# Optimization experiments

Measured on AMD Instinct MI355X. Metric: run time of the kernel, lower is better.

## Reference

```python
import math
import jax, jax.numpy as jnp
import numpy as np

B, LD, LE = 4, 1024, 1024
D, H, DK, DV, DFF, NL = 256, 8, 32, 32, 1024, 6


def _fixed_pos_emb(L, d):
    inv_freq = 1.0 / (10000.0 ** (jnp.arange(0, d, 2, dtype=jnp.float32) / d))
    pos = jnp.arange(L, dtype=jnp.float32)
    s = pos[:, None] * inv_freq[None, :]          # [L, d/2]
    return jnp.concatenate([jnp.sin(s), jnp.cos(s)], axis=-1)  # [L, d]


def _ln(x, g, b, eps=1e-5):
    m = x.mean(-1, keepdims=True)
    v = x.var(-1, keepdims=True)
    return (x - m) / jnp.sqrt(v + eps) * g + b


def _mha(x_q, x_kv, Wq, bq, Wk, bk, Wv, bv, Wo, bo, g, b, mask):
    Bq, Lq, _ = x_q.shape
    q = (x_q @ Wq + bq).reshape(Bq, Lq, H, DK).transpose(0, 2, 1, 3)   # [B,H,Lq,DK]
    k = (x_kv @ Wk + bk).reshape(Bq, -1, H, DK).transpose(0, 2, 1, 3)  # [B,H,Lk,DK]
    v = (x_kv @ Wv + bv).reshape(Bq, -1, H, DV).transpose(0, 2, 1, 3)  # [B,H,Lk,DV]
    scores = jnp.einsum('bhqd,bhkd->bhqk', q, k) / math.sqrt(DK)
    scores = jnp.where(mask[:, None, :, :], -1e9, scores)
    attn = jax.nn.softmax(scores, axis=-1)
    ctx = jnp.einsum('bhqk,bhkd->bhqd', attn, v)
    ctx = ctx.transpose(0, 2, 1, 3).reshape(Bq, Lq, H * DV)
    return _ln(ctx @ Wo + bo + x_q, g, b)


def _ffn(x, W1, b1, W2, b2, g, b):
    h = jax.nn.relu(x @ W1 + b1)   # conv1d k=1 == pointwise linear
    return _ln(h @ W2 + b2 + x, g, b)


def setup_inputs() -> dict:
    key = jax.random.key(0)
    ks = iter(jax.random.split(key, 40))
    def p(shape):
        return jax.random.normal(next(ks), shape, jnp.float32) * 0.02
    inp = {
        'enc_outputs': jax.random.normal(next(ks), (B, LE, D), jnp.float32),
        'dec_inputs': jax.random.normal(next(ks), (B, LD, 3), jnp.float32),
        'enc_masks': jnp.zeros((B, LE), jnp.int32),
        'dec_masks': jnp.zeros((B, LD), jnp.int32),
        'W_tgt': p((3, D)), 'b_tgt': jnp.zeros((D,), jnp.float32),
        'sa_Wq': p((NL, D, H * DK)), 'sa_bq': jnp.zeros((NL, H * DK), jnp.float32),
        'sa_Wk': p((NL, D, H * DK)), 'sa_bk': jnp.zeros((NL, H * DK), jnp.float32),
        'sa_Wv': p((NL, D, H * DV)), 'sa_bv': jnp.zeros((NL, H * DV), jnp.float32),
        'sa_Wo': p((NL, H * DV, D)), 'sa_bo': jnp.zeros((NL, D), jnp.float32),
        'sa_ln_g': jnp.ones((NL, D), jnp.float32), 'sa_ln_b': jnp.zeros((NL, D), jnp.float32),
        'ca_Wq': p((NL, D, H * DK)), 'ca_bq': jnp.zeros((NL, H * DK), jnp.float32),
        'ca_Wk': p((NL, D, H * DK)), 'ca_bk': jnp.zeros((NL, H * DK), jnp.float32),
        'ca_Wv': p((NL, D, H * DV)), 'ca_bv': jnp.zeros((NL, H * DV), jnp.float32),
        'ca_Wo': p((NL, H * DV, D)), 'ca_bo': jnp.zeros((NL, D), jnp.float32),
        'ca_ln_g': jnp.ones((NL, D), jnp.float32), 'ca_ln_b': jnp.zeros((NL, D), jnp.float32),
        'ff_W1': p((NL, D, DFF)), 'ff_b1': jnp.zeros((NL, DFF), jnp.float32),
        'ff_W2': p((NL, DFF, D)), 'ff_b2': jnp.zeros((NL, D), jnp.float32),
        'ff_ln_g': jnp.ones((NL, D), jnp.float32), 'ff_ln_b': jnp.zeros((NL, D), jnp.float32),
    }
    return inp


def reference(enc_outputs, dec_inputs, enc_masks, dec_masks, W_tgt, b_tgt,
              sa_Wq, sa_bq, sa_Wk, sa_bk, sa_Wv, sa_bv, sa_Wo, sa_bo, sa_ln_g, sa_ln_b,
              ca_Wq, ca_bq, ca_Wk, ca_bk, ca_Wv, ca_bv, ca_Wo, ca_bo, ca_ln_g, ca_ln_b,
              ff_W1, ff_b1, ff_W2, ff_b2, ff_ln_g, ff_ln_b):
    x = dec_inputs @ W_tgt + b_tgt                                  # tgt_emb
    pad = dec_masks[:, None, :].astype(bool)                        # [B,1,LD]
    causal = jnp.triu(jnp.ones((LD, LD), bool), 1)[None]            # [1,LD,LD]
    self_mask = pad | causal                                        # [B,LD,LD]
    cross_mask = jnp.broadcast_to(enc_masks[:, None, :].astype(bool), (x.shape[0], LD, LE))
    pe = _fixed_pos_emb(LD, D)[None]                                # [1,LD,D]
    for i in range(NL):
        x = x + pe                                                  # pos emb applied every layer (as in source)
        x = _mha(x, x, sa_Wq[i], sa_bq[i], sa_Wk[i], sa_bk[i], sa_Wv[i], sa_bv[i],
                 sa_Wo[i], sa_bo[i], sa_ln_g[i], sa_ln_b[i], self_mask)
        x = _mha(x, enc_outputs, ca_Wq[i], ca_bq[i], ca_Wk[i], ca_bk[i], ca_Wv[i], ca_bv[i],
                 ca_Wo[i], ca_bo[i], ca_ln_g[i], ca_ln_b[i], cross_mask)
        x = _ffn(x, ff_W1[i], ff_b1[i], ff_W2[i], ff_b2[i], ff_ln_g[i], ff_ln_b[i])
    return x
```

## Files before the change

kernel.cpp:

```cpp
#include <hip/hip_runtime.h>
#include <hip/hip_bf16.h>

#define B_   4
#define LD_  1024
#define LE_  1024
#define D_   256
#define H_   8
#define DK_  32
#define DFF_ 1024
#define NL_  6
#define NTOK (B_ * LD_)
#define M1E  1048576

typedef __hip_bfloat16 bf16;
typedef __bf16 bf16_t;
typedef bf16_t bf16x8 __attribute__((ext_vector_type(8)));
typedef bf16_t bf16x4 __attribute__((ext_vector_type(4)));
typedef float  f32x4  __attribute__((ext_vector_type(4)));

__device__ __forceinline__ float bits2f(unsigned short u) {
    union { unsigned int i; float f; } w; w.i = ((unsigned int)u) << 16; return w.f;
}
__device__ __forceinline__ float ldx(const void* p, size_t i, int f32) {
    if (f32) return ((const float*)p)[i];
    return bits2f(((const unsigned short*)p)[i]);
}

__global__ __launch_bounds__(256) void detect_kernel(
    const void* __restrict__ enc, int* __restrict__ flag)
{
    __shared__ int bad;
    if (threadIdx.x == 0) bad = 0;
    __syncthreads();
    const unsigned short* u = (const unsigned short*)enc;
    int b = 0;
    for (int i = threadIdx.x; i < 4096; i += 256) {
        unsigned short e = (u[i] >> 7) & 0xFF;
        if (e >= 142) b = 1;
    }
    if (b) atomicOr(&bad, 1);
    __syncthreads();
    if (threadIdx.x == 0) *flag = bad;
}

__global__ __launch_bounds__(256) void pe_build_kernel(float* __restrict__ pe)
{
    int i = blockIdx.x * 256 + threadIdx.x;
    int d = i & (D_ - 1);
    int pos = i >> 8;
    int j = d & 127;
    float inv = powf(10000.0f, -2.0f * (float)j / (float)D_);
    float s = (float)pos * inv;
    pe[i] = (d < 128) ? sinf(s) : cosf(s);
}

__global__ __launch_bounds__(256) void embed_kernel(
    const void* __restrict__ dec, const void* __restrict__ Wt,
    const void* __restrict__ bt, float* __restrict__ x,
    const float* __restrict__ pe, const int* __restrict__ flag)
{
    int f32 = *flag;
    int i = blockIdx.x * 256 + threadIdx.x;
    int d = i & (D_ - 1);
    int t = i >> 8;
    float a0 = ldx(dec, t * 3 + 0, f32);
    float a1 = ldx(dec, t * 3 + 1, f32);
    float a2 = ldx(dec, t * 3 + 2, f32);
    x[i] = ldx(bt, d, f32) + a0 * ldx(Wt, 0 * D_ + d, f32)
         + a1 * ldx(Wt, 1 * D_ + d, f32) + a2 * ldx(Wt, 2 * D_ + d, f32)
         + pe[i & (LD_ * D_ - 1)];
}

__global__ __launch_bounds__(256) void conv_kernel(
    const void* __restrict__ in, float* __restrict__ out, const int* __restrict__ flag)
{
    int f32 = *flag;
    int i = blockIdx.x * 256 + threadIdx.x;
    out[i] = ldx(in, i, f32);
}

__global__ __launch_bounds__(256) void gemm3_kernel(
    const float* __restrict__ A0, const float* __restrict__ A1, const float* __restrict__ A2,
    const void* __restrict__ W0, const void* __restrict__ W1, const void* __restrict__ W2,
    const void* __restrict__ bias0, const void* __restrict__ bias1, const void* __restrict__ bias2,
    float* __restrict__ C0, float* __restrict__ C1, float* __restrict__ C2,
    size_t wOff, size_t bOff,
    int M, int N, int K, int relu, int mode, const int* __restrict__ flag)
{
    const int f32 = *flag;
    const int z = blockIdx.z;
    const float* A = (z == 0) ? A0 : (z == 1) ? A1 : A2;
    const void*  W = (z == 0) ? W0 : (z == 1) ? W1 : W2;
    const void*  bias = (z == 0) ? bias0 : (z == 1) ? bias1 : bias2;
    float* C = (z == 0) ? C0 : (z == 1) ? C1 : C2;

    __shared__ __align__(16) bf16_t Ahi[32][40];
    __shared__ __align__(16) bf16_t Alo[32][40];
    __shared__ __align__(16) bf16_t Whi[64][40];
    __shared__ __align__(16) bf16_t Wlo[64][40];

    const int tid = threadIdx.x;
    const int m0 = blockIdx.y * 32, n0 = blockIdx.x * 64;
    const int w = tid >> 6, l = tid & 63, l15 = l & 15, lg = l >> 4;
    const int wr = w >> 1, wc = w & 1;

    const int ar = tid >> 3, ac = (tid & 7) * 4;
    const int wn = tid & 63, wkg = tid >> 6;
    const int wkb = 8 * (wkg ^ ((wn >> 3) & 3));

    const int fa = 16 * wr + l15;
    const int c0 = 32 * wc + l15, c1 = c0 + 16;
    const int kb0 = 8 * (lg ^ ((c0 >> 3) & 3));
    const int kb1 = 8 * (lg ^ ((c1 >> 3) & 3));

    f32x4 acc0 = {0.f, 0.f, 0.f, 0.f};
    f32x4 acc1 = {0.f, 0.f, 0.f, 0.f};

    float4 av = *(const float4*)&A[(size_t)(m0 + ar) * K + ac];
    float wf[8];
#pragma unroll
    for (int j = 0; j < 8; ++j)
        wf[j] = ldx(W, wOff + (size_t)(8 * wkg + j) * N + n0 + wn, f32);

    for (int k0 = 0; k0 < K; k0 += 32) {
        __syncthreads();
        {
            float af[4] = {av.x, av.y, av.z, av.w};
            bf16x4 h4, l4;
#pragma unroll
            for (int j = 0; j < 4; ++j) {
                bf16_t hv = (bf16_t)af[j];
                h4[j] = hv;
                l4[j] = (bf16_t)(af[j] - (float)hv);
            }
            *(bf16x4*)&Ahi[ar][ac] = h4;
            *(bf16x4*)&Alo[ar][ac] = l4;
            bf16x8 h8;
#pragma unroll
            for (int j = 0; j < 8; ++j) h8[j] = (bf16_t)wf[j];
            *(bf16x8*)&Whi[wn][wkb] = h8;
            if (f32) {
                bf16x8 l8;
#pragma unroll
                for (int j = 0; j < 8; ++j) l8[j] = (bf16_t)(wf[j] - (float)((bf16_t)wf[j]));
                *(bf16x8*)&Wlo[wn][wkb] = l8;
            }
        }
        __syncthreads();

        if (k0 + 32 < K) {
            av = *(const float4*)&A[(size_t)(m0 + ar) * K + k0 + 32 + ac];
#pragma unroll
            for (int j = 0; j < 8; ++j)
                wf[j] = ldx(W, wOff + (size_t)(k0 + 32 + 8 * wkg + j) * N + n0 + wn, f32);
        }

        bf16x8 ah = *(const bf16x8*)&Ahi[fa][8 * lg];
        bf16x8 al = *(const bf16x8*)&Alo[fa][8 * lg];
        bf16x8 bh0 = *(const bf16x8*)&Whi[c0][kb0];
        bf16x8 bh1 = *(const bf16x8*)&Whi[c1][kb1];
        acc0 = __builtin_amdgcn_mfma_f32_16x16x32_bf16(ah, bh0, acc0, 0, 0, 0);
        acc0 = __builtin_amdgcn_mfma_f32_16x16x32_bf16(al, bh0, acc0, 0, 0, 0);
        acc1 = __builtin_amdgcn_mfma_f32_16x16x32_bf16(ah, bh1, acc1, 0, 0, 0);
        acc1 = __builtin_amdgcn_mfma_f32_16x16x32_bf16(al, bh1, acc1, 0, 0, 0);
        if (f32) {
            bf16x8 bl0 = *(const bf16x8*)&Wlo[c0][kb0];
            bf16x8 bl1 = *(const bf16x8*)&Wlo[c1][kb1];
            acc0 = __builtin_amdgcn_mfma_f32_16x16x32_bf16(ah, bl0, acc0, 0, 0, 0);
            acc1 = __builtin_amdgcn_mfma_f32_16x16x32_bf16(ah, bl1, acc1, 0, 0, 0);
        }
    }

    const int cm = m0 + 16 * wr + 4 * lg;
    const int cn = n0 + 32 * wc + l15;
    const float b0v = ldx(bias, bOff + cn, f32);
    const float b1v = ldx(bias, bOff + cn + 16, f32);
    if (mode == 0) {
#pragma unroll
        for (int r = 0; r < 4; ++r) {
            float v0 = acc0[r] + b0v;
            float v1 = acc1[r] + b1v;
            if (relu) { v0 = fmaxf(v0, 0.f); v1 = fmaxf(v1, 0.f); }
            C[(size_t)(cm + r) * N + cn]      = v0;
            C[(size_t)(cm + r) * N + cn + 16] = v1;
        }
    } else {
        bf16_t* Cb = (bf16_t*)C;
        const float qs = (z == 0) ? 0.17677669529663687f : 1.0f;
#pragma unroll
        for (int r = 0; r < 4; ++r) {
            const int token = cm + r;
#pragma unroll
            for (int cc = 0; cc < 2; ++cc) {
                const int d = cn + 16 * cc;
                const float v = ((cc == 0 ? acc0[r] : acc1[r]) + (cc == 0 ? b0v : b1v)) * qs;
                if (z < 2) {
                    int bb = token >> 10, qw = (token >> 4) & 63, lt = token & 15;
                    int hh = d >> 5, lg2 = (d >> 3) & 3, jj = d & 7;
                    size_t base = ((size_t)((bb * 8 + hh) * 64 + qw)) * 1024
                                + (size_t)(lg2 * 16 + lt) * 8 + jj;
                    bf16_t hv = (bf16_t)v;
                    Cb[base]       = hv;
                    Cb[base + 512] = (bf16_t)(v - (float)hv);
                } else {
                    int bb = token >> 10, ktt = (token >> 6) & 15, c2 = (token >> 5) & 1;
                    int w32 = token & 31;
                    int lg2 = (w32 >> 2) & 3, jj = (w32 >> 4) * 4 + (w32 & 3);
                    int hh = d >> 5, dvh = (d >> 4) & 1, lt = d & 15;
                    size_t base = ((size_t)((bb * 8 + hh) * 16 + ktt)) * 2048
                                + c2 * 1024 + dvh * 512 + (size_t)(lg2 * 16 + lt) * 8 + jj;
                    Cb[base] = (bf16_t)v;
                }
            }
        }
    }
}

__global__ __launch_bounds__(256) void fattn4_kernel(
    const bf16_t* __restrict__ Qf, const bf16_t* __restrict__ Kf,
    const bf16_t* __restrict__ Vf, float* __restrict__ O,
    const int* __restrict__ mask, int causal)
{
    const int tid = threadIdx.x;
    const int qt = blockIdx.x, h = blockIdx.y, b = blockIdx.z;
    const int w = tid >> 6, l = tid & 63, l15 = l & 15, lg = l >> 4;
    const int bh = b * H_ + h;

    const size_t qbase = ((size_t)(bh * 64 + qt * 4 + w)) * 1024 + l * 8;
    const bf16x8 qh = *(const bf16x8*)(Qf + qbase);
    const bf16x8 ql = *(const bf16x8*)(Qf + qbase + 512);
    const int q_global = qt * 64 + w * 16 + l15;

    const bf16_t* kp = Kf + (size_t)bh * 64 * 1024 + l * 8;
    const bf16_t* vp = Vf + (size_t)bh * 16 * 2048 + l * 8;
    const int*    mp = mask + b * 1024 + 4 * lg;

    float m = -3.0e38f, lsum = 0.0f;
    f32x4 o0 = {0.f, 0.f, 0.f, 0.f};
    f32x4 o1 = {0.f, 0.f, 0.f, 0.f};

    const int nkt = causal ? (qt + 1) : (LE_ / 64);

    bf16x8 kha[4], kla[4], vaa[4];  int4 mka[4];
    bf16x8 khb[4], klb[4], vab[4];  int4 mkb[4];

#define FA_LOAD(kh_, kl_, va_, mk_, KT) do {                                    \
    _Pragma("unroll")                                                           \
    for (int nt = 0; nt < 4; ++nt) {                                            \
        kh_[nt] = *(const bf16x8*)(kp + (size_t)(KT) * 4096 + nt * 1024);       \
        kl_[nt] = *(const bf16x8*)(kp + (size_t)(KT) * 4096 + nt * 1024 + 512); \
    }                                                                           \
    va_[0] = *(const bf16x8*)(vp + (size_t)(KT) * 2048);                        \
    va_[1] = *(const bf16x8*)(vp + (size_t)(KT) * 2048 + 1024);                 \
    va_[2] = *(const bf16x8*)(vp + (size_t)(KT) * 2048 + 512);                  \
    va_[3] = *(const bf16x8*)(vp + (size_t)(KT) * 2048 + 1536);                 \
    _Pragma("unroll")                                                           \
    for (int nt = 0; nt < 4; ++nt)                                              \
        mk_[nt] = *(const int4*)(mp + (KT) * 64 + nt * 16);                     \
} while (0)

#define FA_COMPUTE(kh_, kl_, va_, mk_, KT) do {                                 \
    f32x4 s[4];                                                                 \
    _Pragma("unroll")                                                           \
    for (int nt = 0; nt < 4; ++nt) {                                            \
        f32x4 acc = {0.f, 0.f, 0.f, 0.f};                                       \
        acc = __builtin_amdgcn_mfma_f32_16x16x32_bf16(kh_[nt], qh, acc, 0,0,0); \
        acc = __builtin_amdgcn_mfma_f32_16x16x32_bf16(kl_[nt], qh, acc, 0,0,0); \
        acc = __builtin_amdgcn_mfma_f32_16x16x32_bf16(kh_[nt], ql, acc, 0,0,0); \
        s[nt] = acc;                                                            \
    }                                                                           \
    float pm = -3.0e38f;                                                        \
    _Pragma("unroll")                                                           \
    for (int nt = 0; nt < 4; ++nt) {                                            \
        _Pragma("unroll")                                                       \
        for (int r = 0; r < 4; ++r) {                                           \
            int key = (KT) * 64 + 16 * nt + 4 * lg + r;                         \
            int mv = (r==0)?mk_[nt].x:(r==1)?mk_[nt].y:(r==2)?mk_[nt].z:mk_[nt].w; \
            bool dead = (mv != 0) || (causal && key > q_global);                \
            float v = dead ? -1e30f : s[nt][r];                                 \
            s[nt][r] = v;                                                       \
            pm = fmaxf(pm, v);                                                  \
        }                                                                       \
    }                                                                           \
    pm = fmaxf(pm, __shfl_xor(pm, 16));                                         \
    pm = fmaxf(pm, __shfl_xor(pm, 32));                                         \
    float mnew = fmaxf(m, pm);                                                  \
    float alpha = __expf(m - mnew);                                             \
    m = mnew;                                                                   \
    float psum = 0.f;                                                           \
    _Pragma("unroll")                                                           \
    for (int nt = 0; nt < 4; ++nt) {                                            \
        _Pragma("unroll")                                                       \
        for (int r = 0; r < 4; ++r) {                                           \
            float p = __expf(s[nt][r] - m);                                     \
            s[nt][r] = p;                                                       \
            psum += p;                                                          \
        }                                                                       \
    }                                                                           \
    psum += __shfl_xor(psum, 16);                                               \
    psum += __shfl_xor(psum, 32);                                               \
    lsum = lsum * alpha + psum;                                                 \
    _Pragma("unroll")                                                           \
    for (int r = 0; r < 4; ++r) { o0[r] *= alpha; o1[r] *= alpha; }             \
    bf16x8 pb0, pb1;                                                            \
    _Pragma("unroll")                                                           \
    for (int r = 0; r < 4; ++r) {                                               \
        pb0[r]     = (bf16_t)s[0][r];  pb0[4 + r] = (bf16_t)s[1][r];            \
        pb1[r]     = (bf16_t)s[2][r];  pb1[4 + r] = (bf16_t)s[3][r];            \
    }                                                                           \
    o0 = __builtin_amdgcn_mfma_f32_16x16x32_bf16(va_[0], pb0, o0, 0, 0, 0);     \
    o0 = __builtin_amdgcn_mfma_f32_16x16x32_bf16(va_[1], pb1, o0, 0, 0, 0);     \
    o1 = __builtin_amdgcn_mfma_f32_16x16x32_bf16(va_[2], pb0, o1, 0, 0, 0);     \
    o1 = __builtin_amdgcn_mfma_f32_16x16x32_bf16(va_[3], pb1, o1, 0, 0, 0);     \
} while (0)

    FA_LOAD(kha, kla, vaa, mka, 0);
    int kt = 0;
    for (; kt + 2 <= nkt; kt += 2) {
        FA_LOAD(khb, klb, vab, mkb, kt + 1);
        FA_COMPUTE(kha, kla, vaa, mka, kt);
        if (kt + 2 < nkt) FA_LOAD(kha, kla, vaa, mka, kt + 2);
        FA_COMPUTE(khb, klb, vab, mkb, kt + 1);
    }
    if (kt < nkt) FA_COMPUTE(kha, kla, vaa, mka, kt);

#undef FA_LOAD
#undef FA_COMPUTE

    const float inv = 1.0f / lsum;
    float* op = O + ((size_t)(b * LD_ + q_global)) * D_ + h * DK_ + 4 * lg;
    f32x4 r0, r1;
#pragma unroll
    for (int r = 0; r < 4; ++r) { r0[r] = o0[r] * inv; r1[r] = o1[r] * inv; }
    *(f32x4*)op = r0;
    *(f32x4*)(op + 16) = r1;
}

__global__ __launch_bounds__(256) void ln_res_kernel(
    const float* __restrict__ t, float* __restrict__ x,
    const void* __restrict__ g, const void* __restrict__ bt,
    size_t gbOff, const float* __restrict__ pe, int addpe,
    const int* __restrict__ flag)
{
    int f32 = *flag;
    int tok = blockIdx.x * 4 + (threadIdx.x >> 6);
    int l = threadIdx.x & 63;
    size_t base = (size_t)tok * D_ + 4 * l;
    f32x4 tv = *(const f32x4*)(t + base);
    f32x4 xv = *(const f32x4*)(x + base);
    f32x4 v;
    float s1 = 0.f, s2 = 0.f;
#pragma unroll
    for (int j = 0; j < 4; ++j) {
        v[j] = tv[j] + xv[j];
        s1 += v[j];
        s2 += v[j] * v[j];
    }
#pragma unroll
    for (int off = 1; off < 64; off <<= 1) {
        s1 += __shfl_xor(s1, off);
        s2 += __shfl_xor(s2, off);
    }
    float mean = s1 * (1.0f / 256.0f);
    float var  = s2 * (1.0f / 256.0f) - mean * mean;
    float inv  = 1.0f / sqrtf(var + 1e-5f);
    f32x4 out;
#pragma unroll
    for (int j = 0; j < 4; ++j)
        out[j] = (v[j] - mean) * inv * ldx(g, gbOff + 4 * l + j, f32)
               + ldx(bt, gbOff + 4 * l + j, f32);
    if (addpe) {
        size_t pbase = (size_t)(tok & (LD_ - 1)) * D_ + 4 * l;
        f32x4 pv = *(const f32x4*)(pe + pbase);
#pragma unroll
        for (int j = 0; j < 4; ++j) out[j] += pv[j];
    }
    *(f32x4*)(x + base) = out;
}

__global__ __launch_bounds__(256) void cast_kernel(
    const float* __restrict__ x, void* __restrict__ out, const int* __restrict__ flag)
{
    int f32 = *flag;
    int i = blockIdx.x * 256 + threadIdx.x;
    if (f32) ((float*)out)[i] = x[i];
    else ((bf16*)out)[i] = __float2bfloat16(x[i]);
}

extern "C" void kernel_launch(void* const* d_in, const int* in_sizes, int n_in,
                              void* d_out, int out_size, void* d_ws, size_t ws_size,
                              hipStream_t stream)
{
    const void* enc       = d_in[0];
    const void* dec       = d_in[1];
    const int*  enc_masks = (const int*)d_in[2];
    const int*  dec_masks = (const int*)d_in[3];
    const void* W_tgt = d_in[4];
    const void* b_tgt = d_in[5];
    const void* sa_Wq = d_in[6];
    const void* sa_bq = d_in[7];
    const void* sa_Wk = d_in[8];
    const void* sa_bk = d_in[9];
    const void* sa_Wv = d_in[10];
    const void* sa_bv = d_in[11];
    const void* sa_Wo = d_in[12];
    const void* sa_bo = d_in[13];
    const void* sa_ln_g = d_in[14];
    const void* sa_ln_b = d_in[15];
    const void* ca_Wq = d_in[16];
    const void* ca_bq = d_in[17];
    const void* ca_Wk = d_in[18];
    const void* ca_bk = d_in[19];
    const void* ca_Wv = d_in[20];
    const void* ca_bv = d_in[21];
    const void* ca_Wo = d_in[22];
    const void* ca_bo = d_in[23];
    const void* ca_ln_g = d_in[24];
    const void* ca_ln_b = d_in[25];
    const void* ff_W1 = d_in[26];
    const void* ff_b1 = d_in[27];
    const void* ff_W2 = d_in[28];
    const void* ff_b2 = d_in[29];
    const void* ff_ln_g = d_in[30];
    const void* ff_ln_b = d_in[31];

    const size_t M1 = (size_t)NTOK * D_;
    float* ws = (float*)d_ws;
    float* x     = ws;
    float* t     = ws + 1 * M1;
    float* ctx   = ws + 2 * M1;
    float* enc_f = ws + 3 * M1;
    float* h     = ws + 4 * M1;
    bf16_t* qbuf = (bf16_t*)(ws + 4 * M1);
    bf16_t* kbuf = (bf16_t*)(ws + 5 * M1);
    bf16_t* vtbuf= (bf16_t*)(ws + 6 * M1);
    float* pe    = ws + 8 * M1;
    int*   flag  = (int*)(ws + 9 * M1);

    const int nElem = NTOK * D_;

    detect_kernel<<<1, 256, 0, stream>>>(enc, flag);
    pe_build_kernel<<<(LD_ * D_) / 256, 256, 0, stream>>>(pe);
    embed_kernel<<<nElem / 256, 256, 0, stream>>>(dec, W_tgt, b_tgt, x, pe, flag);
    conv_kernel<<<nElem / 256, 256, 0, stream>>>(enc, enc_f, flag);

    dim3 gProj(D_ / 64, NTOK / 32, 3);
    dim3 gOne(D_ / 64, NTOK / 32, 1);
    dim3 gFF1(DFF_ / 64, NTOK / 32, 1);
    dim3 gAttn(LD_ / 64, H_, B_);

    for (int i = 0; i < NL_; ++i) {
        const size_t wOff  = (size_t)i * D_ * D_;
        const size_t bOff  = (size_t)i * D_;
        const size_t f1Off = (size_t)i * D_ * DFF_;
        const size_t f1bOff= (size_t)i * DFF_;

        gemm3_kernel<<<gProj, 256, 0, stream>>>(
            x, x, x, sa_Wq, sa_Wk, sa_Wv, sa_bq, sa_bk, sa_bv,
            (float*)qbuf, (float*)kbuf, (float*)vtbuf,
            wOff, bOff, NTOK, D_, D_, 0, 1, flag);
        fattn4_kernel<<<gAttn, 256, 0, stream>>>(qbuf, kbuf, vtbuf, ctx, dec_masks, 1);
        gemm3_kernel<<<gOne, 256, 0, stream>>>(
            ctx, ctx, ctx, sa_Wo, sa_Wo, sa_Wo, sa_bo, sa_bo, sa_bo,
            t, t, t, wOff, bOff, NTOK, D_, D_, 0, 0, flag);
        ln_res_kernel<<<NTOK / 4, 256, 0, stream>>>(t, x, sa_ln_g, sa_ln_b, bOff, pe, 0, flag);

        gemm3_kernel<<<gProj, 256, 0, stream>>>(
            x, enc_f, enc_f, ca_Wq, ca_Wk, ca_Wv, ca_bq, ca_bk, ca_bv,
            (float*)qbuf, (float*)kbuf, (float*)vtbuf,
            wOff, bOff, NTOK, D_, D_, 0, 1, flag);
        fattn4_kernel<<<gAttn, 256, 0, stream>>>(qbuf, kbuf, vtbuf, ctx, enc_masks, 0);
        gemm3_kernel<<<gOne, 256, 0, stream>>>(
            ctx, ctx, ctx, ca_Wo, ca_Wo, ca_Wo, ca_bo, ca_bo, ca_bo,
            t, t, t, wOff, bOff, NTOK, D_, D_, 0, 0, flag);
        ln_res_kernel<<<NTOK / 4, 256, 0, stream>>>(t, x, ca_ln_g, ca_ln_b, bOff, pe, 0, flag);

        gemm3_kernel<<<gFF1, 256, 0, stream>>>(
            x, x, x, ff_W1, ff_W1, ff_W1, ff_b1, ff_b1, ff_b1,
            h, h, h, f1Off, f1bOff, NTOK, DFF_, D_, 1, 0, flag);
        gemm3_kernel<<<gOne, 256, 0, stream>>>(
            h, h, h, ff_W2, ff_W2, ff_W2, ff_b2, ff_b2, ff_b2,
            t, t, t, f1Off, bOff, NTOK, D_, DFF_, 0, 0, flag);
        ln_res_kernel<<<NTOK / 4, 256, 0, stream>>>(
            t, x, ff_ln_g, ff_ln_b, bOff, pe, (i < NL_ - 1) ? 1 : 0, flag);
    }

    cast_kernel<<<nElem / 256, 256, 0, stream>>>(x, d_out, flag);
}
```

Measured before the change: 1.100 ms.

## Fuse output projection GEMM with residual LayerNorm; skip A-lo pass for bf16 enc inputs

Adds a gemmln kernel in which each 1024-thread block computes a full 256-wide row tile of 16 tokens. It adds bias and residual and performs the LayerNorm reduction in-kernel, replacing the separate GEMM plus ln_res launches and the round trip through the t buffer. Each block reloads all of W for its K range, and a 16-row tile with 1024 threads may give lower MFMA efficiency than the earlier 32x64 tiles. It also drops the low-order split of the A operand for cross-attention K/V projections when inputs are bf16, since the encoder activations are exactly representable. It swizzles the query-tile order for attention blocks to balance the causal load.

Result: no change. 1.107 ms (+0.6%).

```diff
diff --git a/kernel.cpp b/kernel.cpp
--- a/kernel.cpp
+++ b/kernel.cpp
@@ -85,7 +85,7 @@
     const void* __restrict__ bias0, const void* __restrict__ bias1, const void* __restrict__ bias2,
     float* __restrict__ C0, float* __restrict__ C1, float* __restrict__ C2,
     size_t wOff, size_t bOff,
-    int M, int N, int K, int relu, int mode, const int* __restrict__ flag)
+    int M, int N, int K, int relu, int mode, int aexact, const int* __restrict__ flag)
 {
     const int f32 = *flag;
     const int z = blockIdx.z;
@@ -93,6 +93,7 @@
     const void*  W = (z == 0) ? W0 : (z == 1) ? W1 : W2;
     const void*  bias = (z == 0) ? bias0 : (z == 1) ? bias1 : bias2;
     float* C = (z == 0) ? C0 : (z == 1) ? C1 : C2;
+    const int ax = (!f32 && aexact && z > 0);
 
     __shared__ __align__(16) bf16_t Ahi[32][40];
     __shared__ __align__(16) bf16_t Alo[32][40];
@@ -134,7 +135,7 @@
                 l4[j] = (bf16_t)(af[j] - (float)hv);
             }
             *(bf16x4*)&Ahi[ar][ac] = h4;
-            *(bf16x4*)&Alo[ar][ac] = l4;
+            if (!ax) *(bf16x4*)&Alo[ar][ac] = l4;
             bf16x8 h8;
 #pragma unroll
             for (int j = 0; j < 8; ++j) h8[j] = (bf16_t)wf[j];
@@ -156,13 +157,15 @@
         }
 
         bf16x8 ah = *(const bf16x8*)&Ahi[fa][8 * lg];
-        bf16x8 al = *(const bf16x8*)&Alo[fa][8 * lg];
         bf16x8 bh0 = *(const bf16x8*)&Whi[c0][kb0];
         bf16x8 bh1 = *(const bf16x8*)&Whi[c1][kb1];
         acc0 = __builtin_amdgcn_mfma_f32_16x16x32_bf16(ah, bh0, acc0, 0, 0, 0);
-        acc0 = __builtin_amdgcn_mfma_f32_16x16x32_bf16(al, bh0, acc0, 0, 0, 0);
         acc1 = __builtin_amdgcn_mfma_f32_16x16x32_bf16(ah, bh1, acc1, 0, 0, 0);
-        acc1 = __builtin_amdgcn_mfma_f32_16x16x32_bf16(al, bh1, acc1, 0, 0, 0);
+        if (!ax) {
+            bf16x8 al = *(const bf16x8*)&Alo[fa][8 * lg];
+            acc0 = __builtin_amdgcn_mfma_f32_16x16x32_bf16(al, bh0, acc0, 0, 0, 0);
+            acc1 = __builtin_amdgcn_mfma_f32_16x16x32_bf16(al, bh1, acc1, 0, 0, 0);
+        }
         if (f32) {
             bf16x8 bl0 = *(const bf16x8*)&Wlo[c0][kb0];
             bf16x8 bl1 = *(const bf16x8*)&Wlo[c1][kb1];
@@ -216,13 +219,145 @@
     }
 }
 
+__global__ __launch_bounds__(1024) void gemmln_kernel(
+    const float* __restrict__ A, const void* __restrict__ W,
+    const void* __restrict__ bias, float* __restrict__ x,
+    const void* __restrict__ g, const void* __restrict__ bt,
+    size_t wOff, size_t bOff, int K,
+    const float* __restrict__ pe, int addpe, const int* __restrict__ flag)
+{
+    const int f32 = *flag;
+    __shared__ __align__(16) bf16_t Ahi[16][40];
+    __shared__ __align__(16) bf16_t Alo[16][40];
+    __shared__ __align__(16) bf16_t Whi[256][40];
+    __shared__ __align__(16) bf16_t Wlo[256][40];
+    __shared__ float red1[16][16];
+    __shared__ float red2[16][16];
+    __shared__ float mrow[16], irow[16];
+
+    const int tid = threadIdx.x;
+    const int m0 = blockIdx.x * 16;
+    const int w = tid >> 6, l = tid & 63, l15 = l & 15, lg = l >> 4;
+
+    const int ar = tid >> 3, ac = (tid & 7) * 4;
+    const int wn = tid & 255, wkg = tid >> 8;
+    const int wkb = 8 * (wkg ^ ((wn >> 3) & 3));
+    const int c = 16 * w + l15;
+    const int kb = 8 * (lg ^ ((c >> 3) & 3));
+
+    f32x4 acc = {0.f, 0.f, 0.f, 0.f};
+
+    float4 av;
+    float wf[8];
+    if (tid < 128) av = *(const float4*)&A[(size_t)(m0 + ar) * K + ac];
+#pragma unroll
+    for (int j = 0; j < 8; ++j)
+        wf[j] = ldx(W, wOff + (size_t)(8 * wkg + j) * 256 + wn, f32);
+
+    for (int k0 = 0; k0 < K; k0 += 32) {
+        __syncthreads();
+        if (tid < 128) {
+            float af[4] = {av.x, av.y, av.z, av.w};
+            bf16x4 h4, l4;
+#pragma unroll
+            for (int j = 0; j < 4; ++j) {
+                bf16_t hv = (bf16_t)af[j];
+                h4[j] = hv;
+                l4[j] = (bf16_t)(af[j] - (float)hv);
+            }
+            *(bf16x4*)&Ahi[ar][ac] = h4;
+            *(bf16x4*)&Alo[ar][ac] = l4;
+        }
+        {
+            bf16x8 h8;
+#pragma unroll
+            for (int j = 0; j < 8; ++j) h8[j] = (bf16_t)wf[j];
+            *(bf16x8*)&Whi[wn][wkb] = h8;
+            if (f32) {
+                bf16x8 l8;
+#pragma unroll
+                for (int j = 0; j < 8; ++j) l8[j] = (bf16_t)(wf[j] - (float)((bf16_t)wf[j]));
+                *(bf16x8*)&Wlo[wn][wkb] = l8;
+            }
+        }
+        __syncthreads();
+
+        if (k0 + 32 < K) {
+            if (tid < 128) av = *(const float4*)&A[(size_t)(m0 + ar) * K + k0 + 32 + ac];
+#pragma unroll
+            for (int j = 0; j < 8; ++j)
+                wf[j] = ldx(W, wOff + (size_t)(k0 + 32 + 8 * wkg + j) * 256 + wn, f32);
+        }
+
+        bf16x8 ah = *(const bf16x8*)&Ahi[l15][8 * lg];
+        bf16x8 bh = *(const bf16x8*)&Whi[c][kb];
+        acc = __builtin_amdgcn_mfma_f32_16x16x32_bf16(ah, bh, acc, 0, 0, 0);
+        {
+            bf16x8 al = *(const bf16x8*)&Alo[l15][8 * lg];
+            acc = __builtin_amdgcn_mfma_f32_16x16x32_bf16(al, bh, acc, 0, 0, 0);
+        }
+        if (f32) {
+            bf16x8 bl = *(const bf16x8*)&Wlo[c][kb];
+            acc = __builtin_amdgcn_mfma_f32_16x16x32_bf16(ah, bl, acc, 0, 0, 0);
+        }
+    }
+
+    const float bv = ldx(bias, bOff + c, f32);
+    f32x4 v;
+    float s1[4], s2[4];
+#pragma unroll
+    for (int r = 0; r < 4; ++r) {
+        int tok = m0 + 4 * lg + r;
+        v[r] = acc[r] + bv + x[(size_t)tok * 256 + c];
+        s1[r] = v[r];
+        s2[r] = v[r] * v[r];
+    }
+#pragma unroll
+    for (int r = 0; r < 4; ++r) {
+        s1[r] += __shfl_xor(s1[r], 1);  s2[r] += __shfl_xor(s2[r], 1);
+        s1[r] += __shfl_xor(s1[r], 2);  s2[r] += __shfl_xor(s2[r], 2);
+        s1[r] += __shfl_xor(s1[r], 4);  s2[r] += __shfl_xor(s2[r], 4);
+        s1[r] += __shfl_xor(s1[r], 8);  s2[r] += __shfl_xor(s2[r], 8);
+    }
+    if (l15 == 0) {
+#pragma unroll
+        for (int r = 0; r < 4; ++r) {
+            red1[w][4 * lg + r] = s1[r];
+            red2[w][4 * lg + r] = s2[r];
+        }
+    }
+    __syncthreads();
+    if (tid < 16) {
+        float t1 = 0.f, t2 = 0.f;
+#pragma unroll
+        for (int ww = 0; ww < 16; ++ww) { t1 += red1[ww][tid]; t2 += red2[ww][tid]; }
+        float mean = t1 * (1.0f / 256.0f);
+        float var  = t2 * (1.0f / 256.0f) - mean * mean;
+        mrow[tid] = mean;
+        irow[tid] = 1.0f / sqrtf(var + 1e-5f);
+    }
+    __syncthreads();
+
+    const float gv  = ldx(g,  bOff + c, f32);
+    const float btv = ldx(bt, bOff + c, f32);
+#pragma unroll
+    for (int r = 0; r < 4; ++r) {
+        int row = 4 * lg + r;
+        int tok = m0 + row;
+        float out = (v[r] - mrow[row]) * irow[row] * gv + btv;
+        if (addpe) out += pe[(size_t)(tok & (LD_ - 1)) * 256 + c];
+        x[(size_t)tok * 256 + c] = out;
+    }
+}
+
 __global__ __launch_bounds__(256) void fattn4_kernel(
     const bf16_t* __restrict__ Qf, const bf16_t* __restrict__ Kf,
     const bf16_t* __restrict__ Vf, float* __restrict__ O,
     const int* __restrict__ mask, int causal)
 {
     const int tid = threadIdx.x;
-    const int qt = blockIdx.x, h = blockIdx.y, b = blockIdx.z;
+    const int qt = (int)blockIdx.x ^ ((((int)blockIdx.z >> 1) & 1) << 3);
+    const int h = blockIdx.y, b = blockIdx.z;
     const int w = tid >> 6, l = tid & 63, l15 = l & 15, lg = l >> 4;
     const int bh = b * H_ + h;
 
@@ -334,48 +469,6 @@
     for (int r = 0; r < 4; ++r) { r0[r] = o0[r] * inv; r1[r] = o1[r] * inv; }
     *(f32x4*)op = r0;
     *(f32x4*)(op + 16) = r1;
-}
-
-__global__ __launch_bounds__(256) void ln_res_kernel(
-    const float* __restrict__ t, float* __restrict__ x,
-    const void* __restrict__ g, const void* __restrict__ bt,
-    size_t gbOff, const float* __restrict__ pe, int addpe,
-    const int* __restrict__ flag)
-{
-    int f32 = *flag;
-    int tok = blockIdx.x * 4 + (threadIdx.x >> 6);
-    int l = threadIdx.x & 63;
-    size_t base = (size_t)tok * D_ + 4 * l;
-    f32x4 tv = *(const f32x4*)(t + base);
-    f32x4 xv = *(const f32x4*)(x + base);
-    f32x4 v;
-    float s1 = 0.f, s2 = 0.f;
-#pragma unroll
-    for (int j = 0; j < 4; ++j) {
-        v[j] = tv[j] + xv[j];
-        s1 += v[j];
-        s2 += v[j] * v[j];
-    }
-#pragma unroll
-    for (int off = 1; off < 64; off <<= 1) {
-        s1 += __shfl_xor(s1, off);
-        s2 += __shfl_xor(s2, off);
-    }
-    float mean = s1 * (1.0f / 256.0f);
-    float var  = s2 * (1.0f / 256.0f) - mean * mean;
-    float inv  = 1.0f / sqrtf(var + 1e-5f);
-    f32x4 out;
-#pragma unroll
-    for (int j = 0; j < 4; ++j)
-        out[j] = (v[j] - mean) * inv * ldx(g, gbOff + 4 * l + j, f32)
-               + ldx(bt, gbOff + 4 * l + j, f32);
-    if (addpe) {
-        size_t pbase = (size_t)(tok & (LD_ - 1)) * D_ + 4 * l;
-        f32x4 pv = *(const f32x4*)(pe + pbase);
-#pragma unroll
-        for (int j = 0; j < 4; ++j) out[j] += pv[j];
-    }
-    *(f32x4*)(x + base) = out;
 }
 
 __global__ __launch_bounds__(256) void cast_kernel(
@@ -438,6 +531,7 @@
     int*   flag  = (int*)(ws + 9 * M1);
 
     const int nElem = NTOK * D_;
+    (void)t;
 
     detect_kernel<<<1, 256, 0, stream>>>(enc, flag);
     pe_build_kernel<<<(LD_ * D_) / 256, 256, 0, stream>>>(pe);
@@ -445,7 +539,6 @@
     conv_kernel<<<nElem / 256, 256, 0, stream>>>(enc, enc_f, flag);
 
     dim3 gProj(D_ / 64, NTOK / 32, 3);
-    dim3 gOne(D_ / 64, NTOK / 32, 1);
     dim3 gFF1(DFF_ / 64, NTOK / 32, 1);
     dim3 gAttn(LD_ / 64, H_, B_);
 
@@ -458,31 +551,25 @@
         gemm3_kernel<<<gProj, 256, 0, stream>>>(
             x, x, x, sa_Wq, sa_Wk, sa_Wv, sa_bq, sa_bk, sa_bv,
             (float*)qbuf, (float*)kbuf, (float*)vtbuf,
-            wOff, bOff, NTOK, D_, D_, 0, 1, flag);
+            wOff, bOff, NTOK, D_, D_, 0, 1, 0, flag);
         fattn4_kernel<<<gAttn, 256, 0, stream>>>(qbuf, kbuf, vtbuf, ctx, dec_masks, 1);
-        gemm3_kernel<<<gOne, 256, 0, stream>>>(
-            ctx, ctx, ctx, sa_Wo, sa_Wo, sa_Wo, sa_bo, sa_bo, sa_bo,
-            t, t, t, wOff, bOff, NTOK, D_, D_, 0, 0, flag);
-        ln_res_kernel<<<NTOK / 4, 256, 0, stream>>>(t, x, sa_ln_g, sa_ln_b, bOff, pe, 0, flag);
+        gemmln_kernel<<<NTOK / 16, 1024, 0, stream>>>(
+            ctx, sa_Wo, sa_bo, x, sa_ln_g, sa_ln_b, wOff, bOff, D_, pe, 0, flag);
 
         gemm3_kernel<<<gProj, 256, 0, stream>>>(
             x, enc_f, enc_f, ca_Wq, ca_Wk, ca_Wv, ca_bq, ca_bk, ca_bv,
             (float*)qbuf, (float*)kbuf, (float*)vtbuf,
-            wOff, bOff, NTOK, D_, D_, 0, 1, flag);
+            wOff, bOff, NTOK, D_, D_, 0, 1, 1, flag);
         fattn4_kernel<<<gAttn, 256, 0, stream>>>(qbuf, kbuf, vtbuf, ctx, enc_masks, 0);
-        gemm3_kernel<<<gOne, 256, 0, stream>>>(
-            ctx, ctx, ctx, ca_Wo, ca_Wo, ca_Wo, ca_bo, ca_bo, ca_bo,
-            t, t, t, wOff, bOff, NTOK, D_, D_, 0, 0, flag);
-        ln_res_kernel<<<NTOK / 4, 256, 0, stream>>>(t, x, ca_ln_g, ca_ln_b, bOff, pe, 0, flag);
+        gemmln_kernel<<<NTOK / 16, 1024, 0, stream>>>(
+            ctx, ca_Wo, ca_bo, x, ca_ln_g, ca_ln_b, wOff, bOff, D_, pe, 0, flag);
 
         gemm3_kernel<<<gFF1, 256, 0, stream>>>(
             x, x, x, ff_W1, ff_W1, ff_W1, ff_b1, ff_b1, ff_b1,
-            h, h, h, f1Off, f1bOff, NTOK, DFF_, D_, 1, 0, flag);
-        gemm3_kernel<<<gOne, 256, 0, stream>>>(
-            h, h, h, ff_W2, ff_W2, ff_W2, ff_b2, ff_b2, ff_b2,
-            t, t, t, f1Off, bOff, NTOK, D_, DFF_, 0, 0, flag);
-        ln_res_kernel<<<NTOK / 4, 256, 0, stream>>>(
-            t, x, ff_ln_g, ff_ln_b, bOff, pe, (i < NL_ - 1) ? 1 : 0, flag);
+            h, h, h, f1Off, f1bOff, NTOK, DFF_, D_, 1, 0, 0, flag);
+        gemmln_kernel<<<NTOK / 16, 1024, 0, stream>>>(
+            h, ff_W2, ff_b2, x, ff_ln_g, ff_ln_b, f1Off, bOff, DFF_,
+            pe, (i < NL_ - 1) ? 1 : 0, flag);
     }
 
     cast_kernel<<<nElem / 256, 256, 0, stream>>>(x, d_out, flag);
```
